# Performance work log

Measured on AMD Instinct MI355X. Metric: run time of the kernel, lower is better.

Reference implementation:

```python
import jax, jax.numpy as jnp
import numpy as np

N_NODES = 100000
N_EDGES = 3200000
M = 24
HID = 32
OUT = 16


def neighbor_mean(feat, row, col, num_nodes):
    # sum features of source nodes into destination nodes, divide by in-degree
    sums = jax.ops.segment_sum(feat[row], col, num_segments=num_nodes)  # (N, F)
    deg = jax.ops.segment_sum(jnp.ones_like(col, dtype=feat.dtype), col, num_segments=num_nodes)
    return sums / jnp.clip(deg, 1.0)[:, None]


def sage_conv(x, row, col, num_nodes, w_l, b_l, w_r):
    # PyG SAGEConv(aggr='mean'): lin_l(mean_aggr) + lin_r(x); lin_r has no bias
    aggr = neighbor_mean(x, row, col, num_nodes)
    return aggr @ w_l.T + b_l + x @ w_r.T


def setup_inputs() -> dict:
    key = jax.random.key(0)
    ks = jax.random.split(key, 10)
    x_bin = jax.random.randint(ks[0], (N_NODES, M), 0, 2).astype(jnp.float32)
    edge_index = jax.random.randint(ks[1], (2, N_EDGES), 0, N_NODES).astype(jnp.int64)
    s = 0.1
    return {
        "x_bin": x_bin,
        "edge_index": edge_index,
        "w1l": s * jax.random.normal(ks[2], (HID, M), jnp.float32),
        "b1": s * jax.random.normal(ks[3], (HID,), jnp.float32),
        "w1r": s * jax.random.normal(ks[4], (HID, M), jnp.float32),
        "w2l": s * jax.random.normal(ks[5], (OUT, HID), jnp.float32),
        "b2": s * jax.random.normal(ks[6], (OUT,), jnp.float32),
        "w2r": s * jax.random.normal(ks[7], (OUT, HID), jnp.float32),
        "head_w": s * jax.random.normal(ks[8], (1, 3 * M + OUT), jnp.float32),
        "head_b": s * jax.random.normal(ks[9], (1,), jnp.float32),
    }


def reference(x_bin, edge_index, w1l, b1, w1r, w2l, b2, w2r, head_w, head_b):
    num_nodes = x_bin.shape[0]
    row, col = edge_index[0], edge_index[1]
    # explicit branch: [self markers | neighbor fraction | self * neighbor fraction]
    frac1 = neighbor_mean(x_bin, row, col, num_nodes)
    feats = jnp.concatenate([x_bin, frac1, x_bin * frac1], axis=1)  # (N, 3M)
    # GNN branch: SmallSAGE (dropout is identity at inference)
    h = jax.nn.relu(sage_conv(x_bin, row, col, num_nodes, w1l, b1, w1r))
    emb = jax.nn.relu(sage_conv(h, row, col, num_nodes, w2l, b2, w2r))  # (N, OUT)
    z = jnp.concatenate([feats, emb], axis=1)  # (N, 3M+OUT)
    yhat = (z @ head_w.T + head_b)[:, 0]  # (N,)
    return yhat, z
```

## Files before the change

### kernel.cpp

```cpp
#include <hip/hip_runtime.h>
#include <hip/hip_bf16.h>

#define MF 24
#define HIDF 32
#define OUTF 16
#define ZDIM 88
#define NPB 8
#define NPB2 32
#define SW1 28
#define SW2 36

#define NB 512
#define EB 4096
#define CAP 8192

union bf16x8 {
    float4 v;
    __hip_bfloat16 h[8];
};
union bf16x2u {
    unsigned int u;
    __hip_bfloat16 h[2];
};

__device__ __forceinline__ float ldw(const void* p, size_t i, bool bf16) {
    return bf16 ? __bfloat162float(((const __hip_bfloat16*)p)[i])
                : ((const float*)p)[i];
}

__device__ __forceinline__ bool detect_bf(const unsigned int* __restrict__ xw) {
    unsigned int w = xw[threadIdx.x & 63];
    return __ballot((w & 0xFFFFu) == 0x3F80u) != 0ull;
}
__device__ __forceinline__ bool detect_i64(const unsigned int* __restrict__ ew) {
    unsigned int w = ew[2 * (threadIdx.x & 63) + 1];
    return __popcll(__ballot(w == 0u)) >= 32;
}

__device__ __forceinline__ int bkt_of(int c, unsigned long long Wm) {
    return (int)(((unsigned long long)(unsigned)c * Wm) >> 32);
}

#define HIST_EDGE(c_)                                                   \
    if ((unsigned)(c_) < (unsigned)N) atomicAdd(&hist[bkt_of(c_, Wm)], 1);

__global__ __launch_bounds__(256) void k_histA(
    const void* __restrict__ x, unsigned int* __restrict__ xpack,
    const int* __restrict__ ei, int* __restrict__ counts,
    int nE, int N, unsigned long long Wm) {
    const bool bf16 = detect_bf((const unsigned int*)x);
    const bool i64 = detect_i64((const unsigned int*)ei);

    for (int n = blockIdx.x * 256 + threadIdx.x; n < N; n += gridDim.x * 256) {
        unsigned int m = 0;
        if (bf16) {
            const float4* xr = reinterpret_cast<const float4*>(
                (const __hip_bfloat16*)x + (size_t)n * MF);
            bf16x8 u;
#pragma unroll
            for (int q = 0; q < 3; ++q) {
                u.v = xr[q];
#pragma unroll
                for (int i = 0; i < 8; ++i)
                    if (__bfloat162float(u.h[i]) != 0.f) m |= 1u << (q * 8 + i);
            }
        } else {
            const float* xr = (const float*)x + (size_t)n * MF;
#pragma unroll
            for (int k = 0; k < MF; ++k)
                if (xr[k] != 0.f) m |= 1u << k;
        }
        xpack[n] = m;
    }

    __shared__ int hist[NB];
    for (int i = threadIdx.x; i < NB; i += 256) hist[i] = 0;
    __syncthreads();
    size_t base = (size_t)blockIdx.x * EB;
    int m = nE - (int)base;
    if (m > EB) m = EB;
    if (!(nE & 1)) {
        int nPair = m >> 1;
        if (i64) {
            const int4* cp = (const int4*)ei + (((size_t)nE + base) >> 1);
            for (int j = threadIdx.x; j < nPair; j += 256) {
                int4 c4 = cp[j];
                HIST_EDGE(c4.x);
                HIST_EDGE(c4.z);
            }
        } else {
            const int2* cp = (const int2*)ei + (((size_t)nE + base) >> 1);
            for (int j = threadIdx.x; j < nPair; j += 256) {
                int2 c2 = cp[j];
                HIST_EDGE(c2.x);
                HIST_EDGE(c2.y);
            }
        }
        for (int i = (nPair << 1) + threadIdx.x; i < m; i += 256) {
            size_t e = base + i;
            int c = i64 ? ei[2 * ((size_t)nE + e)] : ei[(size_t)nE + e];
            HIST_EDGE(c);
        }
    } else {
        for (int i = threadIdx.x; i < m; i += 256) {
            size_t e = base + i;
            int c = i64 ? ei[2 * ((size_t)nE + e)] : ei[(size_t)nE + e];
            HIST_EDGE(c);
        }
    }
    __syncthreads();
    for (int i = threadIdx.x; i < NB; i += 256)
        counts[(size_t)blockIdx.x * NB + i] = hist[i];
}

__global__ __launch_bounds__(1024) void k_colscan(int* __restrict__ counts,
                                                  int* __restrict__ colSum, int nBlk) {
    __shared__ int s[1024];
    int b = blockIdx.x, t = threadIdx.x;
    int v = (t < nBlk) ? counts[(size_t)t * NB + b] : 0;
    s[t] = v;
    __syncthreads();
    for (int off = 1; off < 1024; off <<= 1) {
        int y = (t >= off) ? s[t - off] : 0;
        __syncthreads();
        s[t] += y;
        __syncthreads();
    }
    if (t < nBlk) counts[(size_t)t * NB + b] = s[t] - v;
    if (t == 1023) colSum[b] = s[1023];
}

__global__ __launch_bounds__(1024) void k_bstart(const int* __restrict__ colSum,
                                                 int* __restrict__ bucketStart) {
    __shared__ int s[1024];
    int t = threadIdx.x;
    int v = (t < NB) ? colSum[t] : 0;
    s[t] = v;
    __syncthreads();
    for (int off = 1; off < 1024; off <<= 1) {
        int y = (t >= off) ? s[t - off] : 0;
        __syncthreads();
        s[t] += y;
        __syncthreads();
    }
    if (t < NB) bucketStart[t] = s[t] - v;
    if (t == NB - 1) bucketStart[NB] = s[t];
}

#define SCAT_EDGE(r_, c_)                                               \
    if ((unsigned)(c_) < (unsigned)N) {                                 \
        int b_ = bkt_of(c_, Wm);                                        \
        int ld_ = (c_) - b_ * W;                                        \
        unsigned rr_ = ((unsigned)(r_) < (unsigned)N) ? (unsigned)(r_) : 0u; \
        int pos_ = ldsStart[b_] + atomicAdd(&lcnt[b_], 1);              \
        rec[pos_] = rr_ | ((unsigned)ld_ << 20);                        \
        bkt[pos_] = (unsigned short)b_;                                 \
    }

__global__ __launch_bounds__(256) void k_scatB(
    const int* __restrict__ ei, const int* __restrict__ counts,
    const int* __restrict__ colSum, const int* __restrict__ bucketStart,
    unsigned int* __restrict__ part, int nE, int N, int W,
    unsigned long long Wm, int nBlk) {
    const bool i64 = detect_i64((const unsigned int*)ei);
    __shared__ unsigned int rec[EB];
    __shared__ unsigned short bkt[EB];
    __shared__ int ldsStart[NB + 1];
    __shared__ int lcnt[NB];
    __shared__ int base2[NB];
    __shared__ int s256[256];
    const int t = threadIdx.x, blk = blockIdx.x;

    for (int b = t; b < NB; b += 256) {
        int pre = counts[(size_t)blk * NB + b];
        int nxt = (blk + 1 < nBlk) ? counts[(size_t)(blk + 1) * NB + b] : colSum[b];
        ldsStart[b] = nxt - pre;
        lcnt[b] = 0;
        base2[b] = bucketStart[b] + pre;
    }
    __syncthreads();

    int v0 = ldsStart[2 * t], v1 = ldsStart[2 * t + 1];
    int pairSum = v0 + v1;
    s256[t] = pairSum;
    __syncthreads();
    for (int off = 1; off < 256; off <<= 1) {
        int y = (t >= off) ? s256[t - off] : 0;
        __syncthreads();
        s256[t] += y;
        __syncthreads();
    }
    int base = s256[t] - pairSum;
    ldsStart[2 * t] = base;
    ldsStart[2 * t + 1] = base + v0;
    if (t == 255) ldsStart[NB] = base + pairSum;
    __syncthreads();
    for (int b = t; b < NB; b += 256) base2[b] -= ldsStart[b];
    __syncthreads();

    size_t eb = (size_t)blk * EB;
    int m = nE - (int)eb;
    if (m > EB) m = EB;
    if (!(nE & 1)) {
        int nPair = m >> 1;
        if (i64) {
            const int4* rp = (const int4*)ei + (eb >> 1);
            const int4* cp = (const int4*)ei + (((size_t)nE + eb) >> 1);
            for (int j = t; j < nPair; j += 256) {
                int4 r4 = rp[j];
                int4 c4 = cp[j];
                SCAT_EDGE(r4.x, c4.x);
                SCAT_EDGE(r4.z, c4.z);
            }
        } else {
            const int2* rp = (const int2*)ei + (eb >> 1);
            const int2* cp = (const int2*)ei + (((size_t)nE + eb) >> 1);
            for (int j = t; j < nPair; j += 256) {
                int2 r2 = rp[j];
                int2 c2 = cp[j];
                SCAT_EDGE(r2.x, c2.x);
                SCAT_EDGE(r2.y, c2.y);
            }
        }
        for (int i = (nPair << 1) + t; i < m; i += 256) {
            size_t e = eb + i;
            int r = i64 ? ei[2 * e] : ei[e];
            int c = i64 ? ei[2 * ((size_t)nE + e)] : ei[(size_t)nE + e];
            SCAT_EDGE(r, c);
        }
    } else {
        for (int i = t; i < m; i += 256) {
            size_t e = eb + i;
            int r = i64 ? ei[2 * e] : ei[e];
            int c = i64 ? ei[2 * ((size_t)nE + e)] : ei[(size_t)nE + e];
            SCAT_EDGE(r, c);
        }
    }
    __syncthreads();

    int total = ldsStart[NB];
    for (int i = t; i < total; i += 256) {
        int b = bkt[i];
        part[base2[b] + i] = rec[i];
    }
}

__global__ __launch_bounds__(256) void k_csrC(const int* __restrict__ bucketStart,
                                              unsigned int* __restrict__ part,
                                              int* __restrict__ degi,
                                              int* __restrict__ rowstart,
                                              int N, int W) {
    __shared__ unsigned int stage[CAP];
    __shared__ int hist[256];
    __shared__ int sc[256];
    __shared__ int cur[256];
    int b = blockIdx.x, t = threadIdx.x;
    int start = bucketStart[b];
    int bs = bucketStart[b + 1] - start;
    int node = b * W + t;

    hist[t] = 0;
    __syncthreads();

    if (bs > CAP) {
        if (t < W && node < N) { degi[node] = 0; rowstart[node] = start; }
        return;
    }

    for (int i = t; i < bs; i += 256) {
        unsigned int v = part[start + i];
        stage[i] = v;
        atomicAdd(&hist[v >> 20], 1);
    }
    __syncthreads();

    int v = hist[t];
    sc[t] = v;
    __syncthreads();
    for (int off = 1; off < 256; off <<= 1) {
        int y = (t >= off) ? sc[t - off] : 0;
        __syncthreads();
        sc[t] += y;
        __syncthreads();
    }
    int excl = sc[t] - v;
    if (t < W && node < N) {
        degi[node] = v;
        rowstart[node] = start + excl;
    }
    cur[t] = excl;
    __syncthreads();

    for (int i = t; i < bs; i += 256) {
        unsigned int v2 = stage[i];
        int pos = atomicAdd(&cur[v2 >> 20], 1);
        part[start + pos] = v2 & 0xFFFFFu;
    }
}

__device__ __forceinline__ unsigned tstage(unsigned x, unsigned y, unsigned M,
                                           int d, bool hi) {
    return x ^ (hi ? (((y >> d) ^ x) & M) : (((((x >> d) ^ y) & M)) << d));
}

__device__ __forceinline__ unsigned tcol(unsigned x, int lane) {
    unsigned y;
    y = (unsigned)__builtin_amdgcn_ds_swizzle((int)x, 0x401F);
    x = tstage(x, y, 0x0000FFFFu, 16, (lane & 16) != 0);
    y = (unsigned)__builtin_amdgcn_ds_swizzle((int)x, 0x201F);
    x = tstage(x, y, 0x00FF00FFu, 8, (lane & 8) != 0);
    y = (unsigned)__builtin_amdgcn_ds_swizzle((int)x, 0x101F);
    x = tstage(x, y, 0x0F0F0F0Fu, 4, (lane & 4) != 0);
    y = (unsigned)__builtin_amdgcn_ds_swizzle((int)x, 0x081F);
    x = tstage(x, y, 0x33333333u, 2, (lane & 2) != 0);
    y = (unsigned)__builtin_amdgcn_ds_swizzle((int)x, 0x041F);
    x = tstage(x, y, 0x55555555u, 1, (lane & 1) != 0);
    return x;
}

__global__ __launch_bounds__(256) void k_layer1(
    const void* __restrict__ x, const unsigned int* __restrict__ xpack,
    const int* __restrict__ degi, const int* __restrict__ rowstart,
    const unsigned int* __restrict__ srcs, void* __restrict__ out,
    const void* __restrict__ w1l, const void* __restrict__ b1,
    const void* __restrict__ w1r, const void* __restrict__ w2l,
    const void* __restrict__ b2, const void* __restrict__ w2r,
    const void* __restrict__ head_w,
    __hip_bfloat16* __restrict__ hl, __hip_bfloat16* __restrict__ st,
    float* __restrict__ ypart, int N) {
    const bool bf16 = detect_bf((const unsigned int*)x);
    __shared__ float swl[HIDF * SW1];
    __shared__ float swr[HIDF * SW1];
    __shared__ float sb[HIDF];
    __shared__ float s2l[OUTF * SW2];
    __shared__ float s2r[OUTF * SW2];
    __shared__ float sb2[OUTF];
    __shared__ float shw[3 * MF];
    __shared__ float fs[NPB][MF];
    __shared__ float hs[NPB][HIDF];
    for (int i = threadIdx.x; i < HIDF * MF; i += 256) {
        int j = i / MF, k = i - j * MF;
        swl[j * SW1 + k] = ldw(w1l, i, bf16);
        swr[j * SW1 + k] = ldw(w1r, i, bf16);
    }
    for (int i = threadIdx.x; i < OUTF * HIDF; i += 256) {
        int o = i >> 5, j = i & 31;
        s2l[o * SW2 + j] = ldw(w2l, i, bf16);
        s2r[o * SW2 + j] = ldw(w2r, i, bf16);
    }
    if (threadIdx.x < HIDF) sb[threadIdx.x] = ldw(b1, threadIdx.x, bf16);
    if (threadIdx.x < OUTF) sb2[threadIdx.x] = ldw(b2, threadIdx.x, bf16);
    if (threadIdx.x < 3 * MF) shw[threadIdx.x] = ldw(head_w, threadIdx.x, bf16);
    __syncthreads();

    const int lane = threadIdx.x & 31;
    const int wg = threadIdx.x >> 5;
    int node = blockIdx.x * NPB + wg;
    bool valid = node < N;

    int dg = 0, p0 = 0;
    unsigned int xpn = 0;
    if (valid) {
        dg = degi[node];
        p0 = rowstart[node];
        xpn = xpack[node];
    }

    int dgmax = dg;
#pragma unroll
    for (int off = 32; off > 0; off >>= 1)
        dgmax = max(dgmax, __shfl_xor(dgmax, off, 64));

    int cnt = 0;
    for (int base = 0; base < dgmax; base += 128) {
        unsigned int m0 = 0, m1 = 0, m2 = 0, m3 = 0;
        int e0 = base + lane;
        if (e0 < dg) m0 = xpack[srcs[p0 + e0]];
        if (e0 + 32 < dg) m1 = xpack[srcs[p0 + e0 + 32]];
        if (e0 + 64 < dg) m2 = xpack[srcs[p0 + e0 + 64]];
        if (e0 + 96 < dg) m3 = xpack[srcs[p0 + e0 + 96]];
        cnt += __popc(tcol(m0, lane));
        if (base + 32 < dgmax) cnt += __popc(tcol(m1, lane));
        if (base + 64 < dgmax) cnt += __popc(tcol(m2, lane));
        if (base + 96 < dgmax) cnt += __popc(tcol(m3, lane));
    }

    float inv = 1.f / fmaxf((float)dg, 1.f);
    float fv = (float)cnt * inv;
    float xv = (float)((xpn >> lane) & 1);

    float pc = 0.f;
    if (valid && lane < MF) {
        if (bf16) {
            __hip_bfloat16* z = (__hip_bfloat16*)out + N + (size_t)node * ZDIM;
            z[lane] = __float2bfloat16(xv);
            z[MF + lane] = __float2bfloat16(fv);
            z[2 * MF + lane] = __float2bfloat16(xv * fv);
        } else {
            float* z = (float*)out + N + (size_t)node * ZDIM;
            z[lane] = xv;
            z[MF + lane] = fv;
            z[2 * MF + lane] = xv * fv;
        }
        pc = xv * shw[lane] + fv * shw[MF + lane] + xv * fv * shw[2 * MF + lane];
    }

    if (lane < MF) fs[wg][lane] = fv;

    float fvk[MF];
    {
        const float4* fp = (const float4*)fs[wg];
#pragma unroll
        for (int q = 0; q < 6; ++q) {
            float4 f4 = fp[q];
            fvk[q * 4 + 0] = f4.x; fvk[q * 4 + 1] = f4.y;
            fvk[q * 4 + 2] = f4.z; fvk[q * 4 + 3] = f4.w;
        }
    }
    float wlv[MF], wrv[MF];
    {
        const float4* wl4 = (const float4*)(swl + lane * SW1);
        const float4* wr4 = (const float4*)(swr + lane * SW1);
#pragma unroll
        for (int q = 0; q < 6; ++q) {
            float4 a = wl4[q], b = wr4[q];
            wlv[q * 4 + 0] = a.x; wlv[q * 4 + 1] = a.y;
            wlv[q * 4 + 2] = a.z; wlv[q * 4 + 3] = a.w;
            wrv[q * 4 + 0] = b.x; wrv[q * 4 + 1] = b.y;
            wrv[q * 4 + 2] = b.z; wrv[q * 4 + 3] = b.w;
        }
    }
    float acc = sb[lane];
#pragma unroll
    for (int k = 0; k < MF; ++k) {
        acc = fmaf(fvk[k], wlv[k], acc);
        acc += ((xpn >> k) & 1u) ? wrv[k] : 0.f;
    }
    hs[wg][lane] = fmaxf(acc, 0.f);

#pragma unroll
    for (int off = 16; off > 0; off >>= 1) pc += __shfl_down(pc, off, 32);

    int o = lane & 15;
    int half = lane >> 4;
    const float4* wrow4 = (const float4*)((half ? s2r : s2l) + o * SW2);
    const float4* hp4 = (const float4*)hs[wg];
    float d = 0.f;
#pragma unroll
    for (int q = 0; q < 8; ++q) {
        float4 hq = hp4[q], wq = wrow4[q];
        d += hq.x * wq.x + hq.y * wq.y + hq.z * wq.z + hq.w * wq.w;
    }
    if (valid) {
        if (half == 0) hl[(size_t)node * OUTF + o] = __float2bfloat16(d);
        else st[(size_t)node * OUTF + o] = __float2bfloat16(d + sb2[o]);
        if (lane == 0) ypart[node] = pc;
    }
}

__global__ __launch_bounds__(256) void k_layer2(
    const void* __restrict__ x, const int* __restrict__ degi,
    const int* __restrict__ rowstart, const unsigned int* __restrict__ srcs,
    const __hip_bfloat16* __restrict__ hl, const __hip_bfloat16* __restrict__ st,
    const float* __restrict__ ypart, void* __restrict__ out,
    const void* __restrict__ head_w, const void* __restrict__ head_b, int N) {
    const bool bf16 = detect_bf((const unsigned int*)x);
    __shared__ float shw2[OUTF];
    __shared__ float shb;
    if (threadIdx.x < OUTF) shw2[threadIdx.x] = ldw(head_w, 3 * MF + threadIdx.x, bf16);
    if (threadIdx.x == 0) shb = ldw(head_b, 0, bf16);
    __syncthreads();

    int lane = threadIdx.x & 7;
    int g = threadIdx.x >> 3;
    int node = blockIdx.x * NPB2 + g;
    bool valid = node < N;

    int dg = 0, p0 = 0;
    if (valid) {
        dg = degi[node];
        p0 = rowstart[node];
    }
    const unsigned int* hlw = (const unsigned int*)hl;
    float s0 = 0.f, s1 = 0.f;
    int e = 0;
    for (; e + 4 <= dg; e += 4) {
        int a = srcs[p0 + e], b = srcs[p0 + e + 1];
        int c = srcs[p0 + e + 2], d = srcs[p0 + e + 3];
        bf16x2u ua, ub, uc, ud;
        ua.u = hlw[(size_t)a * 8 + lane];
        ub.u = hlw[(size_t)b * 8 + lane];
        uc.u = hlw[(size_t)c * 8 + lane];
        ud.u = hlw[(size_t)d * 8 + lane];
        s0 += (__bfloat162float(ua.h[0]) + __bfloat162float(ub.h[0])) +
              (__bfloat162float(uc.h[0]) + __bfloat162float(ud.h[0]));
        s1 += (__bfloat162float(ua.h[1]) + __bfloat162float(ub.h[1])) +
              (__bfloat162float(uc.h[1]) + __bfloat162float(ud.h[1]));
    }
    for (; e < dg; ++e) {
        bf16x2u ua;
        ua.u = hlw[(size_t)srcs[p0 + e] * 8 + lane];
        s0 += __bfloat162float(ua.h[0]);
        s1 += __bfloat162float(ua.h[1]);
    }

    float emb0 = 0.f, emb1 = 0.f;
    if (valid) {
        float inv = 1.f / fmaxf((float)dg, 1.f);
        bf16x2u us;
        us.u = ((const unsigned int*)st)[(size_t)node * 8 + lane];
        emb0 = fmaxf(s0 * inv + __bfloat162float(us.h[0]), 0.f);
        emb1 = fmaxf(s1 * inv + __bfloat162float(us.h[1]), 0.f);
        if (bf16) {
            __hip_bfloat16* z = (__hip_bfloat16*)out + N + (size_t)node * ZDIM;
            z[3 * MF + 2 * lane] = __float2bfloat16(emb0);
            z[3 * MF + 2 * lane + 1] = __float2bfloat16(emb1);
        } else {
            float* z = (float*)out + N + (size_t)node * ZDIM;
            z[3 * MF + 2 * lane] = emb0;
            z[3 * MF + 2 * lane + 1] = emb1;
        }
    }
    float part = emb0 * shw2[2 * lane] + emb1 * shw2[2 * lane + 1];
#pragma unroll
    for (int off = 4; off > 0; off >>= 1) part += __shfl_down(part, off, 8);
    if (valid && lane == 0) {
        float y = ypart[node] + part + shb;
        if (bf16) ((__hip_bfloat16*)out)[node] = __float2bfloat16(y);
        else ((float*)out)[node] = y;
    }
}

extern "C" void kernel_launch(void* const* d_in, const int* in_sizes, int n_in,
                              void* d_out, int out_size, void* d_ws, size_t ws_size,
                              hipStream_t stream) {
    const void* x = d_in[0];
    const int* ei = (const int*)d_in[1];
    const void* w1l = d_in[2];
    const void* b1 = d_in[3];
    const void* w1r = d_in[4];
    const void* w2l = d_in[5];
    const void* b2 = d_in[6];
    const void* w2r = d_in[7];
    const void* head_w = d_in[8];
    const void* head_b = d_in[9];

    const int N = in_sizes[0] / MF;
    const int nE = in_sizes[1] / 2;
    const int W = (N + NB - 1) / NB;
    const unsigned long long Wm = (0x100000000ull / (unsigned)W) + 1;
    const int nBlkA = (nE + EB - 1) / EB;

    if (N > NB * 256 || N > 131072 || nBlkA > 1024 ||
        (size_t)nBlkA * NB < (size_t)N || nE < 64) return;

    int* bucketStart = (int*)((char*)d_ws + 256);
    int* colSum = bucketStart + (NB + 1);
    int* degi = colSum + NB;
    int* rowstart = degi + N;
    int* counts = rowstart + N;
    unsigned int* part = (unsigned int*)(counts + (size_t)nBlkA * NB);
    unsigned int* xpack = part + nE;
    __hip_bfloat16* hl = (__hip_bfloat16*)(xpack + N);
    __hip_bfloat16* st = hl + (size_t)N * OUTF;
    float* ypart = (float*)counts;

    const size_t need = 256 +
        ((size_t)(NB + 1) + NB + 2 * (size_t)N + (size_t)nBlkA * NB +
         (size_t)nE + (size_t)N) * 4 + (size_t)N * OUTF * 2 * 2;
    if (ws_size < need) return;

    const int gb1 = (N + NPB - 1) / NPB;
    const int gb2 = (N + NPB2 - 1) / NPB2;
    k_histA<<<nBlkA, 256, 0, stream>>>(x, xpack, ei, counts, nE, N, Wm);
    k_colscan<<<NB, 1024, 0, stream>>>(counts, colSum, nBlkA);
    k_bstart<<<1, 1024, 0, stream>>>(colSum, bucketStart);
    k_scatB<<<nBlkA, 256, 0, stream>>>(ei, counts, colSum, bucketStart,
                                       part, nE, N, W, Wm, nBlkA);
    k_csrC<<<NB, 256, 0, stream>>>(bucketStart, part, degi, rowstart, N, W);
    k_layer1<<<gb1, 256, 0, stream>>>(x, xpack, degi, rowstart, part, d_out,
                                      w1l, b1, w1r, w2l, b2, w2r, head_w,
                                      hl, st, ypart, N);
    k_layer2<<<gb2, 256, 0, stream>>>(x, degi, rowstart, part, hl, st, ypart,
                                      d_out, head_w, head_b, N);
}
```

Measured before the change: 235.9 us.

## Fuse neighbor bit-count aggregation into CSR build with packed LDS byte counters

```diff
diff --git a/kernel.cpp b/kernel.cpp
--- a/kernel.cpp
+++ b/kernel.cpp
@@ -249,8 +249,11 @@
                                               unsigned int* __restrict__ part,
                                               int* __restrict__ degi,
                                               int* __restrict__ rowstart,
+                                              const unsigned int* __restrict__ xpack,
+                                              unsigned int* __restrict__ cnt3,
                                               int N, int W) {
     __shared__ unsigned int stage[CAP];
+    __shared__ unsigned int c3[256 * 6];
     __shared__ int hist[256];
     __shared__ int sc[256];
     __shared__ int cur[256];
@@ -260,17 +263,31 @@
     int node = b * W + t;
 
     hist[t] = 0;
+#pragma unroll
+    for (int j = 0; j < 6; ++j) c3[t * 6 + j] = 0;
     __syncthreads();
 
     if (bs > CAP) {
-        if (t < W && node < N) { degi[node] = 0; rowstart[node] = start; }
+        if (t < W && node < N) {
+            degi[node] = 0; rowstart[node] = start;
+#pragma unroll
+            for (int j = 0; j < 6; ++j) cnt3[(size_t)node * 6 + j] = 0;
+        }
         return;
     }
 
     for (int i = t; i < bs; i += 256) {
         unsigned int v = part[start + i];
         stage[i] = v;
-        atomicAdd(&hist[v >> 20], 1);
+        int ld = v >> 20;
+        atomicAdd(&hist[ld], 1);
+        unsigned int xp = xpack[v & 0xFFFFFu];
+        int b3 = ld * 6;
+#pragma unroll
+        for (int j = 0; j < 6; ++j) {
+            unsigned int nib = (xp >> (4 * j)) & 0xFu;
+            atomicAdd(&c3[b3 + j], (nib * 0x00204081u) & 0x01010101u);
+        }
     }
     __syncthreads();
 
@@ -287,6 +304,8 @@
     if (t < W && node < N) {
         degi[node] = v;
         rowstart[node] = start + excl;
+#pragma unroll
+        for (int j = 0; j < 6; ++j) cnt3[(size_t)node * 6 + j] = c3[t * 6 + j];
     }
     cur[t] = excl;
     __syncthreads();
@@ -298,30 +317,10 @@
     }
 }
 
-__device__ __forceinline__ unsigned tstage(unsigned x, unsigned y, unsigned M,
-                                           int d, bool hi) {
-    return x ^ (hi ? (((y >> d) ^ x) & M) : (((((x >> d) ^ y) & M)) << d));
-}
-
-__device__ __forceinline__ unsigned tcol(unsigned x, int lane) {
-    unsigned y;
-    y = (unsigned)__builtin_amdgcn_ds_swizzle((int)x, 0x401F);
-    x = tstage(x, y, 0x0000FFFFu, 16, (lane & 16) != 0);
-    y = (unsigned)__builtin_amdgcn_ds_swizzle((int)x, 0x201F);
-    x = tstage(x, y, 0x00FF00FFu, 8, (lane & 8) != 0);
-    y = (unsigned)__builtin_amdgcn_ds_swizzle((int)x, 0x101F);
-    x = tstage(x, y, 0x0F0F0F0Fu, 4, (lane & 4) != 0);
-    y = (unsigned)__builtin_amdgcn_ds_swizzle((int)x, 0x081F);
-    x = tstage(x, y, 0x33333333u, 2, (lane & 2) != 0);
-    y = (unsigned)__builtin_amdgcn_ds_swizzle((int)x, 0x041F);
-    x = tstage(x, y, 0x55555555u, 1, (lane & 1) != 0);
-    return x;
-}
-
 __global__ __launch_bounds__(256) void k_layer1(
     const void* __restrict__ x, const unsigned int* __restrict__ xpack,
-    const int* __restrict__ degi, const int* __restrict__ rowstart,
-    const unsigned int* __restrict__ srcs, void* __restrict__ out,
+    const int* __restrict__ degi, const unsigned int* __restrict__ cnt3,
+    void* __restrict__ out,
     const void* __restrict__ w1l, const void* __restrict__ b1,
     const void* __restrict__ w1r, const void* __restrict__ w2l,
     const void* __restrict__ b2, const void* __restrict__ w2r,
@@ -358,32 +357,15 @@
     int node = blockIdx.x * NPB + wg;
     bool valid = node < N;
 
-    int dg = 0, p0 = 0;
+    int dg = 0;
     unsigned int xpn = 0;
+    unsigned int cw = 0;
     if (valid) {
         dg = degi[node];
-        p0 = rowstart[node];
         xpn = xpack[node];
-    }
-
-    int dgmax = dg;
-#pragma unroll
-    for (int off = 32; off > 0; off >>= 1)
-        dgmax = max(dgmax, __shfl_xor(dgmax, off, 64));
-
-    int cnt = 0;
-    for (int base = 0; base < dgmax; base += 128) {
-        unsigned int m0 = 0, m1 = 0, m2 = 0, m3 = 0;
-        int e0 = base + lane;
-        if (e0 < dg) m0 = xpack[srcs[p0 + e0]];
-        if (e0 + 32 < dg) m1 = xpack[srcs[p0 + e0 + 32]];
-        if (e0 + 64 < dg) m2 = xpack[srcs[p0 + e0 + 64]];
-        if (e0 + 96 < dg) m3 = xpack[srcs[p0 + e0 + 96]];
-        cnt += __popc(tcol(m0, lane));
-        if (base + 32 < dgmax) cnt += __popc(tcol(m1, lane));
-        if (base + 64 < dgmax) cnt += __popc(tcol(m2, lane));
-        if (base + 96 < dgmax) cnt += __popc(tcol(m3, lane));
-    }
+        if (lane < MF) cw = cnt3[(size_t)node * 6 + (lane >> 2)];
+    }
+    int cnt = (cw >> ((lane & 3) * 8)) & 0xFF;
 
     float inv = 1.f / fmaxf((float)dg, 1.f);
     float fv = (float)cnt * inv;
@@ -512,13 +494,15 @@
         emb0 = fmaxf(s0 * inv + __bfloat162float(us.h[0]), 0.f);
         emb1 = fmaxf(s1 * inv + __bfloat162float(us.h[1]), 0.f);
         if (bf16) {
-            __hip_bfloat16* z = (__hip_bfloat16*)out + N + (size_t)node * ZDIM;
-            z[3 * MF + 2 * lane] = __float2bfloat16(emb0);
-            z[3 * MF + 2 * lane + 1] = __float2bfloat16(emb1);
+            bf16x2u up;
+            up.h[0] = __float2bfloat16(emb0);
+            up.h[1] = __float2bfloat16(emb1);
+            unsigned int* zw = (unsigned int*)((__hip_bfloat16*)out + N +
+                                               (size_t)node * ZDIM + 3 * MF);
+            zw[lane] = up.u;
         } else {
-            float* z = (float*)out + N + (size_t)node * ZDIM;
-            z[3 * MF + 2 * lane] = emb0;
-            z[3 * MF + 2 * lane + 1] = emb1;
+            float2* zw = (float2*)((float*)out + N + (size_t)node * ZDIM + 3 * MF);
+            zw[lane] = make_float2(emb0, emb1);
         }
     }
     float part = emb0 * shw2[2 * lane] + emb1 * shw2[2 * lane + 1];
@@ -563,11 +547,12 @@
     unsigned int* xpack = part + nE;
     __hip_bfloat16* hl = (__hip_bfloat16*)(xpack + N);
     __hip_bfloat16* st = hl + (size_t)N * OUTF;
+    unsigned int* cnt3 = (unsigned int*)(st + (size_t)N * OUTF);
     float* ypart = (float*)counts;
 
     const size_t need = 256 +
         ((size_t)(NB + 1) + NB + 2 * (size_t)N + (size_t)nBlkA * NB +
-         (size_t)nE + (size_t)N) * 4 + (size_t)N * OUTF * 2 * 2;
+         (size_t)nE + (size_t)N + 6 * (size_t)N) * 4 + (size_t)N * OUTF * 2 * 2;
     if (ws_size < need) return;
 
     const int gb1 = (N + NPB - 1) / NPB;
@@ -577,8 +562,9 @@
     k_bstart<<<1, 1024, 0, stream>>>(colSum, bucketStart);
     k_scatB<<<nBlkA, 256, 0, stream>>>(ei, counts, colSum, bucketStart,
                                        part, nE, N, W, Wm, nBlkA);
-    k_csrC<<<NB, 256, 0, stream>>>(bucketStart, part, degi, rowstart, N, W);
-    k_layer1<<<gb1, 256, 0, stream>>>(x, xpack, degi, rowstart, part, d_out,
+    k_csrC<<<NB, 256, 0, stream>>>(bucketStart, part, degi, rowstart,
+                                   xpack, cnt3, N, W);
+    k_layer1<<<gb1, 256, 0, stream>>>(x, xpack, degi, cnt3, d_out,
                                       w1l, b1, w1r, w2l, b2, w2r, head_w,
                                       hl, st, ypart, N);
     k_layer2<<<gb2, 256, 0, stream>>>(x, degi, rowstart, part, hl, st, ypart,
```

Result: no change. 232.0 us (-1.6%).
